# Kernel optimization log

Measured on AMD Instinct MI355X. Metric: run time of the kernel, lower is better.

The kernel has to match this reference:

```python
import jax, jax.numpy as jnp
import numpy as np
import math

DIM = 512
HEADS = 8
B = 16
P = 2048
REL_MAX = 64
REL_SIZE = 2 * REL_MAX + 1
RANK = 4
ALPHA = 16.0
QBITS = 4


def simq(w, bits=QBITS):
    # symmetric linear fake-quantization (matches simulate_quantization)
    qmin = -2 ** (bits - 1)
    qmax = 2 ** (bits - 1) - 1
    m = jnp.max(jnp.abs(w))
    scale = m / qmax
    q = jnp.clip(jnp.round(w / (scale + 1e-8)), qmin, qmax) * scale
    return jnp.where(m == 0, w, q)


def lora_lin(x, W, b, A, LB):
    # F.linear with quantized weight/bias + LoRA path
    out = x @ simq(W).T + simq(b)
    return out + (x @ A.T @ LB.T) * (ALPHA / RANK)


def setup_inputs() -> dict:
    key = jax.random.key(0)
    ks = jax.random.split(key, 20)
    d2 = DIM * 2
    inp = {
        "curr_pos": 2048,
        "z_curr_ri": jax.random.normal(ks[0], (B, DIM, 2), jnp.float32),
        "z_past_ri": jax.random.normal(ks[1], (P, B, DIM, 2), jnp.float32),
        "rel_bias_ri": jax.random.normal(ks[2], (REL_SIZE, DIM, 2), jnp.float32) * 0.02,
    }
    names = ["q", "k", "v", "o"]
    for i, n in enumerate(names):
        kw, ka, kb = jax.random.split(ks[3 + i], 3)
        inp["W" + n] = jax.random.normal(kw, (d2, d2), jnp.float32) / math.sqrt(d2)
        inp["b" + n] = jnp.zeros((d2,), jnp.float32)
        inp["A" + n] = jax.random.normal(ka, (RANK, d2), jnp.float32) / math.sqrt(d2)
        inp["LB" + n] = jax.random.normal(kb, (d2, RANK), jnp.float32) * 0.01
    return inp


def reference(curr_pos, z_curr_ri, z_past_ri, rel_bias_ri,
              Wq, bq, Aq, LBq, Wk, bk, Ak, LBk,
              Wv, bv, Av, LBv, Wo, bo, Ao, LBo):
    Bsz = z_curr_ri.shape[0]
    past_len = z_past_ri.shape[0]
    dim = z_curr_ri.shape[1]
    hd = dim // HEADS

    # projections on real-view of complex inputs ([.., dim, 2] -> [.., 2*dim])
    q = lora_lin(z_curr_ri.reshape(Bsz, dim * 2), Wq, bq, Aq, LBq)
    k = lora_lin(z_past_ri.reshape(past_len, Bsz, dim * 2), Wk, bk, Ak, LBk)
    v = lora_lin(z_past_ri.reshape(past_len, Bsz, dim * 2), Wv, bv, Av, LBv)

    q = q.reshape(Bsz, HEADS, hd, 2)            # [B,H,hd,2]
    k = k.reshape(past_len, Bsz, HEADS, hd, 2)  # [P,B,H,hd,2]
    v = v.reshape(past_len, Bsz, HEADS, hd, 2)
    qr, qi = q[..., 0], q[..., 1]
    kr, ki = k[..., 0], k[..., 1]
    vr, vi = v[..., 0], v[..., 1]

    # Re(q * conj(k)) summed over head_dim -> [B,H,P]
    dot = jnp.einsum('bhd,pbhd->bhp', qr, kr) + jnp.einsum('bhd,pbhd->bhp', qi, ki)

    # relative positional bias lookup (clamped index)
    rel_d = jnp.arange(curr_pos - past_len, curr_pos)
    idx = jnp.clip(rel_d + REL_MAX, 0, rel_bias_ri.shape[0] - 1)
    rb = rel_bias_ri[idx].reshape(past_len, HEADS, hd, 2)  # [P,H,hd,2]
    rel = jnp.einsum('bhd,phd->bhp', qr, rb[..., 0]) + jnp.einsum('bhd,phd->bhp', qi, rb[..., 1])

    w = jax.nn.softmax((dot + rel) / math.sqrt(hd), axis=-1)  # [B,H,P]

    # real softmax weights applied to complex values
    out_r = jnp.einsum('bhp,pbhd->bhd', w, vr)
    out_i = jnp.einsum('bhp,pbhd->bhd', w, vi)
    out_ri = jnp.stack([out_r, out_i], axis=-1).reshape(Bsz, dim * 2)

    o = lora_lin(out_ri, Wo, bo, Ao, LBo)
    return o.reshape(Bsz, dim, 2)  # real view of complex output [B,dim]
```

## Files before the change

kernel.cpp:

```cpp
#include <hip/hip_runtime.h>
#include <math.h>

typedef _Float16 f16;
typedef _Float16 f16x8 __attribute__((ext_vector_type(8)));
typedef _Float16 f16x4 __attribute__((ext_vector_type(4)));
typedef float f32x4 __attribute__((ext_vector_type(4)));

#define NP 2048
#define M_ROWS 32768

#define OFF_ABSMAX 0u
#define OFF_TQ     256u
#define OFF_TO     512u
#define OFF_QBIAS  1024u
#define OFF_QBUF   163840u
#define OFF_ATT    229376u
#define OFF_PM     294912u
#define OFF_PL     299008u
#define OFF_PO     303104u
#define OFF_WH     1048576u
#define OFF_TK     9437184u
#define OFF_TV     9961472u
#define OFF_KV     10485760u

__device__ __forceinline__ float qint_of(float w, float scale) {
    return fminf(7.f, fmaxf(-8.f, rintf(w / (scale + 1e-8f))));
}

__device__ __forceinline__ void gload16(const void* g, void* l) {
  __builtin_amdgcn_global_load_lds((const __attribute__((address_space(1))) void*)g,
                                   (__attribute__((address_space(3))) void*)l, 16, 0, 0);
}

__global__ void __launch_bounds__(256) absmax_kernel(
    const float* __restrict__ W0, const float* __restrict__ W1,
    const float* __restrict__ W2, const float* __restrict__ W3,
    unsigned* __restrict__ absmax) {
  int mat = blockIdx.x >> 6;
  int blk = blockIdx.x & 63;
  const float* W = mat == 0 ? W0 : mat == 1 ? W1 : mat == 2 ? W2 : W3;
  int tid = blk * 256 + threadIdx.x;
  const float4* W4 = (const float4*)W;
  float m = 0.f;
  #pragma unroll
  for (int i = 0; i < 16; ++i) {
    float4 v = W4[tid + i * 16384];
    m = fmaxf(m, fmaxf(fmaxf(fabsf(v.x), fabsf(v.y)), fmaxf(fabsf(v.z), fabsf(v.w))));
  }
  #pragma unroll
  for (int k = 32; k >= 1; k >>= 1) m = fmaxf(m, __shfl_xor(m, k));
  __shared__ float sm[4];
  if ((threadIdx.x & 63) == 0) sm[threadIdx.x >> 6] = m;
  __syncthreads();
  if (threadIdx.x == 0) {
    m = fmaxf(fmaxf(sm[0], sm[1]), fmaxf(sm[2], sm[3]));
    atomicMax(&absmax[mat], __float_as_uint(m));
  }
}

__global__ void __launch_bounds__(256) bias_quant_kernel(
    const float* __restrict__ b0, const float* __restrict__ b1,
    const float* __restrict__ b2, const float* __restrict__ b3,
    float* __restrict__ qbias) {
  int mat = blockIdx.x;
  const float* bb = mat == 0 ? b0 : mat == 1 ? b1 : mat == 2 ? b2 : b3;
  int t = threadIdx.x;
  float4 v = ((const float4*)bb)[t];
  float m = fmaxf(fmaxf(fabsf(v.x), fabsf(v.y)), fmaxf(fabsf(v.z), fabsf(v.w)));
  #pragma unroll
  for (int k = 32; k >= 1; k >>= 1) m = fmaxf(m, __shfl_xor(m, k));
  __shared__ float sm[4];
  if ((t & 63) == 0) sm[t >> 6] = m;
  __syncthreads();
  float M = fmaxf(fmaxf(sm[0], sm[1]), fmaxf(sm[2], sm[3]));
  float scale = M * (1.0f / 7.0f);
  float4 q;
  q.x = (M == 0.f) ? v.x : qint_of(v.x, scale) * scale;
  q.y = (M == 0.f) ? v.y : qint_of(v.y, scale) * scale;
  q.z = (M == 0.f) ? v.z : qint_of(v.z, scale) * scale;
  q.w = (M == 0.f) ? v.w : qint_of(v.w, scale) * scale;
  ((float4*)(qbias + mat * 1024))[t] = q;
}

__global__ void __launch_bounds__(256) quantW_kernel(
    const float* __restrict__ W0, const float* __restrict__ W1,
    const float* __restrict__ W2, const float* __restrict__ W3,
    const unsigned* __restrict__ absmax, f16* __restrict__ Wh,
    f16* __restrict__ WD) {
  int gid = blockIdx.x * 256 + threadIdx.x;
  int mat = gid >> 18;
  int idx = gid & 262143;
  const float* W = mat == 0 ? W0 : mat == 1 ? W1 : mat == 2 ? W2 : W3;
  float scale = __uint_as_float(absmax[mat]) * (1.0f / 7.0f);
  float4 v = ((const float4*)W)[idx];
  f16x4 r;
  r[0] = (f16)qint_of(v.x, scale);
  r[1] = (f16)qint_of(v.y, scale);
  r[2] = (f16)qint_of(v.z, scale);
  r[3] = (f16)qint_of(v.w, scale);
  *(f16x4*)(Wh + (size_t)mat * 1048576 + (size_t)idx * 4) = r;
  if (WD != nullptr && (mat == 1 || mat == 2)) {
    f16x8 d = {r[0], r[0], r[1], r[1], r[2], r[2], r[3], r[3]};
    int n = idx >> 8, c4 = idx & 255;
    *(f16x8*)(WD + (size_t)(mat - 1) * 2097152 + (size_t)n * 2048 + c4 * 8) = d;
  }
}

__global__ void __launch_bounds__(256) lora_t_small_kernel(
    const float* __restrict__ x, const float* __restrict__ A, float* __restrict__ t) {
  int tt = threadIdx.x;
  int b = tt >> 4;
  int r = (tt >> 2) & 3;
  int s = tt & 3;
  const float4* xv = (const float4*)(x + b * 1024 + s * 256);
  const float4* av = (const float4*)(A + r * 1024 + s * 256);
  float acc = 0.f;
  #pragma unroll 4
  for (int i = 0; i < 64; ++i) {
    float4 a = xv[i], c = av[i];
    acc += a.x * c.x + a.y * c.y + a.z * c.z + a.w * c.w;
  }
  acc += __shfl_xor(acc, 1);
  acc += __shfl_xor(acc, 2);
  if (s == 0) t[b * 4 + r] = acc;
}

__global__ void __launch_bounds__(256) lora_t_big_kernel(
    const float* __restrict__ zp, const float* __restrict__ Ak,
    const float* __restrict__ Av, float* __restrict__ tk, float* __restrict__ tv,
    f16* __restrict__ zpi) {
  __shared__ float sA[8 * 1024];
  for (int i = 0; i < 8; ++i) {
    int f4 = threadIdx.x + i * 256;
    float4 v = (f4 < 1024) ? ((const float4*)Ak)[f4] : ((const float4*)Av)[f4 - 1024];
    ((float4*)sA)[f4] = v;
  }
  __syncthreads();
  int lane = threadIdx.x & 63, wave = threadIdx.x >> 6;
  for (int it = 0; it < 4; ++it) {
    int m = blockIdx.x * 16 + wave * 4 + it;
    const float4* xr = (const float4*)(zp + (size_t)m * 1024);
    float acc[8] = {0.f, 0.f, 0.f, 0.f, 0.f, 0.f, 0.f, 0.f};
    for (int c = lane; c < 256; c += 64) {
      float4 xv = xr[c];
      if (zpi) {
        f16 h0 = (f16)xv.x, h1 = (f16)xv.y, h2 = (f16)xv.z, h3 = (f16)xv.w;
        f16x8 iv = {h0, (f16)(xv.x - (float)h0), h1, (f16)(xv.y - (float)h1),
                    h2, (f16)(xv.z - (float)h2), h3, (f16)(xv.w - (float)h3)};
        *(f16x8*)(zpi + (size_t)m * 2048 + c * 8) = iv;
      }
      #pragma unroll
      for (int r = 0; r < 8; ++r) {
        float4 a = ((const float4*)sA)[r * 256 + c];
        acc[r] += xv.x * a.x + xv.y * a.y + xv.z * a.z + xv.w * a.w;
      }
    }
    #pragma unroll
    for (int k = 32; k >= 1; k >>= 1) {
      #pragma unroll
      for (int r = 0; r < 8; ++r) acc[r] += __shfl_xor(acc[r], k);
    }
    if (lane == 0) {
      tk[m * 4 + 0] = acc[0]; tk[m * 4 + 1] = acc[1];
      tk[m * 4 + 2] = acc[2]; tk[m * 4 + 3] = acc[3];
      tv[m * 4 + 0] = acc[4]; tv[m * 4 + 1] = acc[5];
      tv[m * 4 + 2] = acc[6]; tv[m * 4 + 3] = acc[7];
    }
  }
}

__global__ void __launch_bounds__(256) gemv_mfma_kernel(
    const float* __restrict__ x, const f16* __restrict__ Wm,
    const unsigned* __restrict__ absmax, int mat,
    const float* __restrict__ qb, const float* __restrict__ t,
    const float* __restrict__ LB, float* __restrict__ out) {
  int wave = threadIdx.x >> 6, lane = threadIdx.x & 63;
  int nf = blockIdx.x * 4 + wave;
  int n0 = nf * 16;
  int row = lane & 15, kq = lane >> 4;
  f32x4 acc = {0.f, 0.f, 0.f, 0.f};
  const float* xp = x + row * 1024 + kq * 8;
  const f16* wp = Wm + (size_t)(n0 + row) * 1024 + kq * 8;
  #pragma unroll 4
  for (int k0 = 0; k0 < 1024; k0 += 32) {
    float4 a0 = *(const float4*)(xp + k0);
    float4 a1 = *(const float4*)(xp + k0 + 4);
    f16 h0 = (f16)a0.x, h1 = (f16)a0.y, h2 = (f16)a0.z, h3 = (f16)a0.w;
    f16 h4 = (f16)a1.x, h5 = (f16)a1.y, h6 = (f16)a1.z, h7 = (f16)a1.w;
    f16x8 ah = {h0, h1, h2, h3, h4, h5, h6, h7};
    f16x8 al = {(f16)(a0.x - (float)h0), (f16)(a0.y - (float)h1),
                (f16)(a0.z - (float)h2), (f16)(a0.w - (float)h3),
                (f16)(a1.x - (float)h4), (f16)(a1.y - (float)h5),
                (f16)(a1.z - (float)h6), (f16)(a1.w - (float)h7)};
    f16x8 bb = *(const f16x8*)(wp + k0);
    acc = __builtin_amdgcn_mfma_f32_16x16x32_f16(ah, bb, acc, 0, 0, 0);
    acc = __builtin_amdgcn_mfma_f32_16x16x32_f16(al, bb, acc, 0, 0, 0);
  }
  float scale = __uint_as_float(absmax[mat]) * (1.0f / 7.0f);
  int col = n0 + row;
  float bias = qb[col];
  float4 lb = *(const float4*)(LB + col * 4);
  #pragma unroll
  for (int j = 0; j < 4; ++j) {
    int m = kq * 4 + j;
    float4 tvv = *(const float4*)(t + m * 4);
    out[m * 1024 + col] =
        scale * acc[j] + bias + 4.0f * (tvv.x * lb.x + tvv.y * lb.y + tvv.z * lb.z + tvv.w * lb.w);
  }
}

__global__ void __launch_bounds__(256, 2) kv_gemm_kernel(
    const float* __restrict__ zp, const f16* __restrict__ Wh,
    const unsigned* __restrict__ absmax, const float* __restrict__ qbias,
    const float* __restrict__ tk, const float* __restrict__ tv,
    const float* __restrict__ LBk, const float* __restrict__ LBv,
    f16* __restrict__ kout, f16* __restrict__ vout) {
  __shared__ __align__(16) f16 sAh[128][40];
  __shared__ __align__(16) f16 sAl[128][40];
  __shared__ __align__(16) f16 sB[128][40];
  __shared__ float sT[128][4];

  int nb = blockIdx.x;
  int m0 = blockIdx.y * 128;
  bool is_v = nb >= 8;
  int n0 = (nb & 7) * 128;
  int mat = is_v ? 2 : 1;
  const f16* Wm = Wh + (size_t)mat * 1048576;
  const float* ttv = is_v ? tv : tk;
  const float* LBm = is_v ? LBv : LBk;
  const float* qb = qbias + mat * 1024;
  f16* outp = is_v ? vout : kout;

  int tid = threadIdx.x;
  int lane = tid & 63, wave = tid >> 6;
  int wm = (wave >> 1) * 64, wn = (wave & 1) * 64;
  int row = lane & 15, kq = lane >> 4;

  f32x4 acc[4][4];
  #pragma unroll
  for (int i = 0; i < 4; ++i)
    #pragma unroll
    for (int j = 0; j < 4; ++j) acc[i][j] = (f32x4){0.f, 0.f, 0.f, 0.f};

  int sr = tid >> 1, seg = tid & 1;
  const float* asrc = zp + (size_t)(m0 + sr) * 1024 + seg * 16;
  const f16* bsrc = Wm + (size_t)(n0 + sr) * 1024 + seg * 16;

  for (int k0 = 0; k0 < 1024; k0 += 32) {
    __syncthreads();
    float xs[16];
    const float4* a4 = (const float4*)(asrc + k0);
    *(float4*)&xs[0] = a4[0];
    *(float4*)&xs[4] = a4[1];
    *(float4*)&xs[8] = a4[2];
    *(float4*)&xs[12] = a4[3];
    f16 hs[16], ls[16];
    #pragma unroll
    for (int i = 0; i < 16; ++i) {
      f16 h = (f16)xs[i];
      hs[i] = h;
      ls[i] = (f16)(xs[i] - (float)h);
    }
    *(f16x8*)&sAh[sr][seg * 16] = *(f16x8*)&hs[0];
    *(f16x8*)&sAh[sr][seg * 16 + 8] = *(f16x8*)&hs[8];
    *(f16x8*)&sAl[sr][seg * 16] = *(f16x8*)&ls[0];
    *(f16x8*)&sAl[sr][seg * 16 + 8] = *(f16x8*)&ls[8];
    const f16x8* b8 = (const f16x8*)(bsrc + k0);
    *(f16x8*)&sB[sr][seg * 16] = b8[0];
    *(f16x8*)&sB[sr][seg * 16 + 8] = b8[1];
    __syncthreads();
    f16x8 ah[4], al[4], bf[4];
    #pragma unroll
    for (int mi = 0; mi < 4; ++mi) {
      ah[mi] = *(const f16x8*)&sAh[wm + mi * 16 + row][kq * 8];
      al[mi] = *(const f16x8*)&sAl[wm + mi * 16 + row][kq * 8];
    }
    #pragma unroll
    for (int ni = 0; ni < 4; ++ni) bf[ni] = *(const f16x8*)&sB[wn + ni * 16 + row][kq * 8];
    #pragma unroll
    for (int mi = 0; mi < 4; ++mi)
      #pragma unroll
      for (int ni = 0; ni < 4; ++ni)
        acc[mi][ni] = __builtin_amdgcn_mfma_f32_16x16x32_f16(ah[mi], bf[ni], acc[mi][ni], 0, 0, 0);
    #pragma unroll
    for (int mi = 0; mi < 4; ++mi)
      #pragma unroll
      for (int ni = 0; ni < 4; ++ni)
        acc[mi][ni] = __builtin_amdgcn_mfma_f32_16x16x32_f16(al[mi], bf[ni], acc[mi][ni], 0, 0, 0);
  }
  ((float2*)sT)[tid] = ((const float2*)(ttv + (size_t)m0 * 4))[tid];
  __syncthreads();
  float scale = __uint_as_float(absmax[mat]) * (1.0f / 7.0f);
  #pragma unroll
  for (int ni = 0; ni < 4; ++ni) {
    int ncol = n0 + wn + ni * 16 + row;
    int h = ncol >> 7, d = ncol & 127;
    float4 lb = *(const float4*)(LBm + ncol * 4);
    float bias = qb[ncol];
    #pragma unroll
    for (int mi = 0; mi < 4; ++mi) {
      #pragma unroll
      for (int j = 0; j < 4; ++j) {
        int mloc = wm + mi * 16 + kq * 4 + j;
        int m = m0 + mloc;
        int p = m >> 4, b = m & 15;
        float4 t4 = *(const float4*)&sT[mloc][0];
        float val = scale * acc[mi][ni][j] + bias +
                    4.0f * (t4.x * lb.x + t4.y * lb.y + t4.z * lb.z + t4.w * lb.w);
        outp[(((size_t)(b * 8 + h)) * 2048 + p) * 128 + d] = (f16)val;
      }
    }
  }
}

__global__ void __launch_bounds__(256, 2) kv_gemm_fast_kernel(
    const f16* __restrict__ zpi, const f16* __restrict__ WD,
    const unsigned* __restrict__ absmax, const float* __restrict__ qbias,
    const float* __restrict__ tk, const float* __restrict__ tv,
    const float* __restrict__ LBk, const float* __restrict__ LBv,
    f16* __restrict__ kout, f16* __restrict__ vout) {
  __shared__ __align__(16) f16 sbuf[32768];
  __shared__ float sT[128][4];

  int linear = blockIdx.x + (blockIdx.y << 4);
  int xcd = linear & 7;
  int slot = linear >> 3;
  int nb = slot & 15;
  int g = ((slot >> 4) << 3) + xcd;
  int m0 = g << 7;

  bool is_v = nb >= 8;
  int n0 = (nb & 7) * 128;
  int mat = is_v ? 2 : 1;
  int h = nb & 7;
  const float* ttv = is_v ? tv : tk;
  const float* LBm = is_v ? LBv : LBk;
  const float* qb = qbias + mat * 1024;
  f16* outp = is_v ? vout : kout;

  int tid = threadIdx.x;
  int lane = tid & 63, wave = tid >> 6;
  int wm = (wave >> 1) * 64, wn = (wave & 1) * 64;
  int row = lane & 15, kq = lane >> 4;

  const f16* srcA = zpi + (size_t)m0 * 2048;
  const f16* srcB = WD + (size_t)(is_v ? 1 : 0) * 2097152 + (size_t)n0 * 2048;

  int goff[4], lbase[4];
  #pragma unroll
  for (int r = 0; r < 4; ++r) {
    int L = r * 256 + tid;
    int rw = L >> 3, cc = L & 7, cs = cc ^ (rw & 7);
    goff[r] = rw * 2048 + cs * 8;
    lbase[r] = r * 2048 + wave * 512;
  }

  f32x4 acc[4][4];
  #pragma unroll
  for (int i = 0; i < 4; ++i)
    #pragma unroll
    for (int j = 0; j < 4; ++j) acc[i][j] = (f32x4){0.f, 0.f, 0.f, 0.f};

  int radA[8], radB[8];
  #pragma unroll
  for (int mi = 0; mi < 4; ++mi) {
    int Ra = wm + mi * 16 + row;
    int Rb = wn + mi * 16 + row;
    #pragma unroll
    for (int ks = 0; ks < 2; ++ks) {
      radA[mi * 2 + ks] = Ra * 64 + (((ks * 4 + kq) ^ (Ra & 7)) << 3);
      radB[mi * 2 + ks] = Rb * 64 + (((ks * 4 + kq) ^ (Rb & 7)) << 3);
    }
  }

  #pragma unroll
  for (int r = 0; r < 4; ++r) {
    gload16(srcA + goff[r], sbuf + lbase[r]);
    gload16(srcB + goff[r], sbuf + 8192 + lbase[r]);
  }
  __syncthreads();

  int cur = 0;
  for (int t = 0; t < 32; ++t) {
    if (t < 31) {
      int nxt = (cur ^ 1) * 16384;
      int gk = (t + 1) * 64;
      #pragma unroll
      for (int r = 0; r < 4; ++r) {
        gload16(srcA + goff[r] + gk, sbuf + nxt + lbase[r]);
        gload16(srcB + goff[r] + gk, sbuf + nxt + 8192 + lbase[r]);
      }
    }
    const f16* bA = sbuf + cur * 16384;
    const f16* bB = bA + 8192;
    f16x8 af[8], bf[8];
    #pragma unroll
    for (int i = 0; i < 8; ++i) {
      af[i] = *(const f16x8*)&bA[radA[i]];
      bf[i] = *(const f16x8*)&bB[radB[i]];
    }
    #pragma unroll
    for (int ks = 0; ks < 2; ++ks)
      #pragma unroll
      for (int mi = 0; mi < 4; ++mi)
        #pragma unroll
        for (int ni = 0; ni < 4; ++ni)
          acc[mi][ni] = __builtin_amdgcn_mfma_f32_16x16x32_f16(
              af[mi * 2 + ks], bf[ni * 2 + ks], acc[mi][ni], 0, 0, 0);
    __syncthreads();
    cur ^= 1;
  }

  ((float2*)sT)[tid] = ((const float2*)(ttv + (size_t)m0 * 4))[tid];
  __syncthreads();
  float scale = __uint_as_float(absmax[mat]) * (1.0f / 7.0f);
  float biasv[4];
  float4 lbv[4];
  #pragma unroll
  for (int ni = 0; ni < 4; ++ni) {
    int ncol = n0 + wn + ni * 16 + row;
    biasv[ni] = qb[ncol];
    lbv[ni] = *(const float4*)(LBm + ncol * 4);
  }
  float* tbuf = (float*)sbuf;
  int lh = lane >> 5, l5 = lane & 31;
  #pragma unroll
  for (int halfsel = 0; halfsel < 2; ++halfsel) {
    __syncthreads();
    if ((wave >> 1) == halfsel) {
      #pragma unroll
      for (int ni = 0; ni < 4; ++ni) {
        #pragma unroll
        for (int mi = 0; mi < 4; ++mi) {
          #pragma unroll
          for (int j = 0; j < 4; ++j) {
            int ml = mi * 16 + kq * 4 + j;
            float4 t4 = *(const float4*)&sT[wm + ml][0];
            tbuf[ml * 132 + wn + ni * 16 + row] =
                scale * acc[mi][ni][j] + biasv[ni] +
                4.0f * (t4.x * lbv[ni].x + t4.y * lbv[ni].y + t4.z * lbv[ni].z +
                        t4.w * lbv[ni].w);
          }
        }
      }
    }
    __syncthreads();
    #pragma unroll
    for (int it = 0; it < 8; ++it) {
      int ml = it * 8 + wave * 2 + lh;
      int m = m0 + halfsel * 64 + ml;
      int p = m >> 4, b = m & 15;
      float4 v = *(const float4*)&tbuf[ml * 132 + l5 * 4];
      f16x4 hv = {(f16)v.x, (f16)v.y, (f16)v.z, (f16)v.w};
      *(f16x4*)(outp + (((size_t)(b * 8 + h)) * 2048 + p) * 128 + l5 * 4) = hv;
    }
  }
}

__device__ __forceinline__ float4 ld4h(const f16* p) {
  f16x4 v = *reinterpret_cast<const f16x4*>(p);
  return make_float4((float)v[0], (float)v[1], (float)v[2], (float)v[3]);
}

__global__ void __launch_bounds__(256) attn_part_kernel(
    const float* __restrict__ qbuf, const f16* __restrict__ kbuf,
    const f16* __restrict__ vbuf, const float* __restrict__ rel_bias,
    const int* __restrict__ curr_pos_p, float* __restrict__ m_part,
    float* __restrict__ l_part, float* __restrict__ o_part) {
  __shared__ float sS[256];
  __shared__ float red[8];
  __shared__ float sOv[8][132];
  int bh = blockIdx.x;
  int c = blockIdx.y;
  int b = bh >> 3, h = bh & 7;
  int p0 = c * 256;
  int tid = threadIdx.x, lane = tid & 63, wave = tid >> 6;
  int j4 = lane & 31, ph = lane >> 5;
  float4 qv = *(const float4*)(qbuf + b * 1024 + h * 128 + j4 * 4);
  int off = *curr_pos_p - NP + 64;
  const f16* kb = kbuf + ((size_t)bh * 2048 + p0) * 128;
  for (int i = 0; i < 32; ++i) {
    int pl = i * 8 + wave * 2 + ph;
    float4 kv = ld4h(kb + (size_t)pl * 128 + j4 * 4);
    int idx = min(max(p0 + pl + off, 0), 128);
    float4 rb = *(const float4*)(rel_bias + idx * 1024 + h * 128 + j4 * 4);
    float a = qv.x * (kv.x + rb.x) + qv.y * (kv.y + rb.y) +
              qv.z * (kv.z + rb.z) + qv.w * (kv.w + rb.w);
    a += __shfl_xor(a, 16);
    a += __shfl_xor(a, 8);
    a += __shfl_xor(a, 4);
    a += __shfl_xor(a, 2);
    a += __shfl_xor(a, 1);
    if (j4 == 0) sS[pl] = a * 0.125f;
  }
  __syncthreads();
  float v = sS[tid];
  float mx = v;
  #pragma unroll
  for (int k = 32; k >= 1; k >>= 1) mx = fmaxf(mx, __shfl_xor(mx, k));
  if (lane == 0) red[wave] = mx;
  __syncthreads();
  mx = fmaxf(fmaxf(red[0], red[1]), fmaxf(red[2], red[3]));
  float e = expf(v - mx);
  sS[tid] = e;
  float sum = e;
  #pragma unroll
  for (int k = 32; k >= 1; k >>= 1) sum += __shfl_xor(sum, k);
  if (lane == 0) red[4 + wave] = sum;
  __syncthreads();
  float l = red[4] + red[5] + red[6] + red[7];
  int d4 = tid & 31, pg = tid >> 5;
  const f16* vb = vbuf + ((size_t)bh * 2048 + p0 + pg * 32) * 128;
  float4 a4 = make_float4(0.f, 0.f, 0.f, 0.f);
  #pragma unroll 4
  for (int i = 0; i < 32; ++i) {
    float s = sS[pg * 32 + i];
    float4 vv = ld4h(vb + (size_t)i * 128 + d4 * 4);
    a4.x += s * vv.x;
    a4.y += s * vv.y;
    a4.z += s * vv.z;
    a4.w += s * vv.w;
  }
  *(float4*)&sOv[pg][d4 * 4] = a4;
  __syncthreads();
  if (tid < 128) {
    float o = 0.f;
    #pragma unroll
    for (int gI = 0; gI < 8; ++gI) o += sOv[gI][tid];
    int pc = bh * 8 + c;
    o_part[pc * 128 + tid] = o;
    if (tid == 0) {
      m_part[pc] = mx;
      l_part[pc] = l;
    }
  }
}

__global__ void __launch_bounds__(128) attn_combine_kernel(
    const float* __restrict__ m_part, const float* __restrict__ l_part,
    const float* __restrict__ o_part, float* __restrict__ attout) {
  int bh = blockIdx.x;
  int d = threadIdx.x;
  float M = -1e30f;
  #pragma unroll
  for (int c = 0; c < 8; ++c) M = fmaxf(M, m_part[bh * 8 + c]);
  float L = 0.f, o = 0.f;
  #pragma unroll
  for (int c = 0; c < 8; ++c) {
    float w = expf(m_part[bh * 8 + c] - M);
    L += w * l_part[bh * 8 + c];
    o += w * o_part[(bh * 8 + c) * 128 + d];
  }
  int b = bh >> 3, h = bh & 7;
  attout[b * 1024 + h * 128 + d] = o / L;
}

extern "C" void kernel_launch(void* const* d_in, const int* in_sizes, int n_in,
                              void* d_out, int out_size, void* d_ws, size_t ws_size,
                              hipStream_t stream) {
  const int* curr_pos = (const int*)d_in[0];
  const float* z_curr = (const float*)d_in[1];
  const float* z_past = (const float*)d_in[2];
  const float* rel_bias = (const float*)d_in[3];
  const float* Wq = (const float*)d_in[4];
  const float* bq = (const float*)d_in[5];
  const float* Aq = (const float*)d_in[6];
  const float* LBq = (const float*)d_in[7];
  const float* Wk = (const float*)d_in[8];
  const float* bk = (const float*)d_in[9];
  const float* Ak = (const float*)d_in[10];
  const float* LBk = (const float*)d_in[11];
  const float* Wv = (const float*)d_in[12];
  const float* bv = (const float*)d_in[13];
  const float* Av = (const float*)d_in[14];
  const float* LBv = (const float*)d_in[15];
  const float* Wo = (const float*)d_in[16];
  const float* bo = (const float*)d_in[17];
  const float* Ao = (const float*)d_in[18];
  const float* LBo = (const float*)d_in[19];

  char* ws = (char*)d_ws;
  unsigned* absmax = (unsigned*)(ws + OFF_ABSMAX);
  float* t_q = (float*)(ws + OFF_TQ);
  float* t_o = (float*)(ws + OFF_TO);
  float* qbias = (float*)(ws + OFF_QBIAS);
  float* qbuf = (float*)(ws + OFF_QBUF);
  float* attout = (float*)(ws + OFF_ATT);
  float* pm = (float*)(ws + OFF_PM);
  float* pl = (float*)(ws + OFF_PL);
  float* po = (float*)(ws + OFF_PO);
  f16* Wh = (f16*)(ws + OFF_WH);
  float* t_k = (float*)(ws + OFF_TK);
  float* t_v = (float*)(ws + OFF_TV);
  char* kvbase = ws + OFF_KV;

  f16* kb = (f16*)kvbase;
  f16* vb = (f16*)(kvbase + 67108864ull);
  f16* zpi = (f16*)(kvbase + 134217728ull);
  f16* WD = (f16*)(kvbase + 268435456ull);
  bool fast = ws_size >= (size_t)OFF_KV + 276824064ull;

  hipMemsetAsync(absmax, 0, 16, stream);
  absmax_kernel<<<256, 256, 0, stream>>>(Wq, Wk, Wv, Wo, absmax);
  bias_quant_kernel<<<4, 256, 0, stream>>>(bq, bk, bv, bo, qbias);
  quantW_kernel<<<4096, 256, 0, stream>>>(Wq, Wk, Wv, Wo, absmax, Wh,
                                          fast ? WD : nullptr);
  lora_t_small_kernel<<<1, 256, 0, stream>>>(z_curr, Aq, t_q);
  gemv_mfma_kernel<<<16, 256, 0, stream>>>(z_curr, Wh, absmax, 0, qbias, t_q, LBq, qbuf);
  lora_t_big_kernel<<<2048, 256, 0, stream>>>(z_past, Ak, Av, t_k, t_v,
                                              fast ? zpi : nullptr);
  if (fast)
    kv_gemm_fast_kernel<<<dim3(16, 256), 256, 0, stream>>>(
        zpi, WD, absmax, qbias, t_k, t_v, LBk, LBv, kb, vb);
  else
    kv_gemm_kernel<<<dim3(16, 256), 256, 0, stream>>>(
        z_past, Wh, absmax, qbias, t_k, t_v, LBk, LBv, kb, vb);
  attn_part_kernel<<<dim3(128, 8), 256, 0, stream>>>(
      qbuf, kb, vb, rel_bias, curr_pos, pm, pl, po);
  attn_combine_kernel<<<128, 128, 0, stream>>>(pm, pl, po, attout);
  lora_t_small_kernel<<<1, 256, 0, stream>>>(attout, Ao, t_o);
  gemv_mfma_kernel<<<16, 256, 0, stream>>>(attout, Wh + 3ull * 1048576ull, absmax, 3,
                                           qbias + 3 * 1024, t_o, LBo, (float*)d_out);
}
```

Baseline: 753.0 us.

## Split z_past into hi/lo planes and use 32x32 MFMA with 128x256 KV tiles

```diff
diff --git a/kernel.cpp b/kernel.cpp
--- a/kernel.cpp
+++ b/kernel.cpp
@@ -5,6 +5,7 @@
 typedef _Float16 f16x8 __attribute__((ext_vector_type(8)));
 typedef _Float16 f16x4 __attribute__((ext_vector_type(4)));
 typedef float f32x4 __attribute__((ext_vector_type(4)));
+typedef float f32x16 __attribute__((ext_vector_type(16)));
 
 #define NP 2048
 #define M_ROWS 32768
@@ -85,8 +86,7 @@
 __global__ void __launch_bounds__(256) quantW_kernel(
     const float* __restrict__ W0, const float* __restrict__ W1,
     const float* __restrict__ W2, const float* __restrict__ W3,
-    const unsigned* __restrict__ absmax, f16* __restrict__ Wh,
-    f16* __restrict__ WD) {
+    const unsigned* __restrict__ absmax, f16* __restrict__ Wh) {
   int gid = blockIdx.x * 256 + threadIdx.x;
   int mat = gid >> 18;
   int idx = gid & 262143;
@@ -99,11 +99,6 @@
   r[2] = (f16)qint_of(v.z, scale);
   r[3] = (f16)qint_of(v.w, scale);
   *(f16x4*)(Wh + (size_t)mat * 1048576 + (size_t)idx * 4) = r;
-  if (WD != nullptr && (mat == 1 || mat == 2)) {
-    f16x8 d = {r[0], r[0], r[1], r[1], r[2], r[2], r[3], r[3]};
-    int n = idx >> 8, c4 = idx & 255;
-    *(f16x8*)(WD + (size_t)(mat - 1) * 2097152 + (size_t)n * 2048 + c4 * 8) = d;
-  }
 }
 
 __global__ void __launch_bounds__(256) lora_t_small_kernel(
@@ -128,7 +123,7 @@
 __global__ void __launch_bounds__(256) lora_t_big_kernel(
     const float* __restrict__ zp, const float* __restrict__ Ak,
     const float* __restrict__ Av, float* __restrict__ tk, float* __restrict__ tv,
-    f16* __restrict__ zpi) {
+    f16* __restrict__ zph, f16* __restrict__ zpl) {
   __shared__ float sA[8 * 1024];
   for (int i = 0; i < 8; ++i) {
     int f4 = threadIdx.x + i * 256;
@@ -143,11 +138,13 @@
     float acc[8] = {0.f, 0.f, 0.f, 0.f, 0.f, 0.f, 0.f, 0.f};
     for (int c = lane; c < 256; c += 64) {
       float4 xv = xr[c];
-      if (zpi) {
+      if (zph) {
         f16 h0 = (f16)xv.x, h1 = (f16)xv.y, h2 = (f16)xv.z, h3 = (f16)xv.w;
-        f16x8 iv = {h0, (f16)(xv.x - (float)h0), h1, (f16)(xv.y - (float)h1),
-                    h2, (f16)(xv.z - (float)h2), h3, (f16)(xv.w - (float)h3)};
-        *(f16x8*)(zpi + (size_t)m * 2048 + c * 8) = iv;
+        f16x4 hv = {h0, h1, h2, h3};
+        f16x4 lv = {(f16)(xv.x - (float)h0), (f16)(xv.y - (float)h1),
+                    (f16)(xv.z - (float)h2), (f16)(xv.w - (float)h3)};
+        *(f16x4*)(zph + (size_t)m * 1024 + c * 4) = hv;
+        *(f16x4*)(zpl + (size_t)m * 1024 + c * 4) = lv;
       }
       #pragma unroll
       for (int r = 0; r < 8; ++r) {
@@ -314,25 +311,25 @@
 }
 
 __global__ void __launch_bounds__(256, 2) kv_gemm_fast_kernel(
-    const f16* __restrict__ zpi, const f16* __restrict__ WD,
-    const unsigned* __restrict__ absmax, const float* __restrict__ qbias,
-    const float* __restrict__ tk, const float* __restrict__ tv,
-    const float* __restrict__ LBk, const float* __restrict__ LBv,
-    f16* __restrict__ kout, f16* __restrict__ vout) {
+    const f16* __restrict__ zph, const f16* __restrict__ zpl,
+    const f16* __restrict__ Wh, const unsigned* __restrict__ absmax,
+    const float* __restrict__ qbias, const float* __restrict__ tk,
+    const float* __restrict__ tv, const float* __restrict__ LBk,
+    const float* __restrict__ LBv, f16* __restrict__ kout, f16* __restrict__ vout) {
   __shared__ __align__(16) f16 sbuf[32768];
   __shared__ float sT[128][4];
 
-  int linear = blockIdx.x + (blockIdx.y << 4);
+  int linear = blockIdx.x + (blockIdx.y << 3);
   int xcd = linear & 7;
-  int slot = linear >> 3;
-  int nb = slot & 15;
-  int g = ((slot >> 4) << 3) + xcd;
+  int q = linear >> 3;
+  int nb = q & 7;
+  int g = ((q >> 3) << 3) + xcd;
   int m0 = g << 7;
 
-  bool is_v = nb >= 8;
-  int n0 = (nb & 7) * 128;
+  bool is_v = nb >= 4;
+  int n0 = (nb & 3) * 256;
   int mat = is_v ? 2 : 1;
-  int h = nb & 7;
+  const f16* Wm = Wh + (size_t)mat * 1048576;
   const float* ttv = is_v ? tv : tk;
   const float* LBm = is_v ? LBv : LBk;
   const float* qb = qbias + mat * 1024;
@@ -340,73 +337,90 @@
 
   int tid = threadIdx.x;
   int lane = tid & 63, wave = tid >> 6;
-  int wm = (wave >> 1) * 64, wn = (wave & 1) * 64;
-  int row = lane & 15, kq = lane >> 4;
-
-  const f16* srcA = zpi + (size_t)m0 * 2048;
-  const f16* srcB = WD + (size_t)(is_v ? 1 : 0) * 2097152 + (size_t)n0 * 2048;
-
-  int goff[4], lbase[4];
+  int wm = (wave & 1) * 64;
+  int wn = (wave >> 1) * 128;
+  int l31 = lane & 31, kh = lane >> 5;
+
+  const f16* srcAh = zph + (size_t)m0 * 1024;
+  const f16* srcAl = zpl + (size_t)m0 * 1024;
+  const f16* srcB = Wm + (size_t)n0 * 1024;
+
+  int gA[2], gB[4];
+  #pragma unroll
+  for (int r = 0; r < 2; ++r) {
+    int L = r * 256 + tid;
+    gA[r] = (L & 127) * 1024 + (L >> 7) * 8;
+  }
   #pragma unroll
   for (int r = 0; r < 4; ++r) {
     int L = r * 256 + tid;
-    int rw = L >> 3, cc = L & 7, cs = cc ^ (rw & 7);
-    goff[r] = rw * 2048 + cs * 8;
-    lbase[r] = r * 2048 + wave * 512;
-  }
-
-  f32x4 acc[4][4];
-  #pragma unroll
-  for (int i = 0; i < 4; ++i)
-    #pragma unroll
-    for (int j = 0; j < 4; ++j) acc[i][j] = (f32x4){0.f, 0.f, 0.f, 0.f};
-
-  int radA[8], radB[8];
-  #pragma unroll
-  for (int mi = 0; mi < 4; ++mi) {
-    int Ra = wm + mi * 16 + row;
-    int Rb = wn + mi * 16 + row;
-    #pragma unroll
-    for (int ks = 0; ks < 2; ++ks) {
-      radA[mi * 2 + ks] = Ra * 64 + (((ks * 4 + kq) ^ (Ra & 7)) << 3);
-      radB[mi * 2 + ks] = Rb * 64 + (((ks * 4 + kq) ^ (Rb & 7)) << 3);
-    }
-  }
-
-  #pragma unroll
-  for (int r = 0; r < 4; ++r) {
-    gload16(srcA + goff[r], sbuf + lbase[r]);
-    gload16(srcB + goff[r], sbuf + 8192 + lbase[r]);
-  }
+    gB[r] = (L & 255) * 1024 + (L >> 8) * 8;
+  }
+  int ldsA = wave * 512;
+  int ldsB = wave * 512;
+
+  f32x16 acc[2][4];
+  #pragma unroll
+  for (int i = 0; i < 2; ++i)
+    #pragma unroll
+    for (int j = 0; j < 4; ++j)
+      #pragma unroll
+      for (int e = 0; e < 16; ++e) acc[i][j][e] = 0.f;
+
+  int radA[2][2], radB[4][2];
+  #pragma unroll
+  for (int ks = 0; ks < 2; ++ks) {
+    int c = ks * 2 + kh;
+    #pragma unroll
+    for (int ri = 0; ri < 2; ++ri)
+      radA[ri][ks] = (c * 128 + wm + ri * 32 + l31) * 8;
+    #pragma unroll
+    for (int ci = 0; ci < 4; ++ci)
+      radB[ci][ks] = 8192 + (c * 256 + wn + ci * 32 + l31) * 8;
+  }
+
+  #pragma unroll
+  for (int r = 0; r < 2; ++r) {
+    gload16(srcAh + gA[r], sbuf + r * 2048 + ldsA);
+    gload16(srcAl + gA[r], sbuf + 4096 + r * 2048 + ldsA);
+  }
+  #pragma unroll
+  for (int r = 0; r < 4; ++r) gload16(srcB + gB[r], sbuf + 8192 + r * 2048 + ldsB);
   __syncthreads();
 
   int cur = 0;
   for (int t = 0; t < 32; ++t) {
     if (t < 31) {
       int nxt = (cur ^ 1) * 16384;
-      int gk = (t + 1) * 64;
-      #pragma unroll
-      for (int r = 0; r < 4; ++r) {
-        gload16(srcA + goff[r] + gk, sbuf + nxt + lbase[r]);
-        gload16(srcB + goff[r] + gk, sbuf + nxt + 8192 + lbase[r]);
+      int gk = (t + 1) * 32;
+      #pragma unroll
+      for (int r = 0; r < 2; ++r) {
+        gload16(srcAh + gA[r] + gk, sbuf + nxt + r * 2048 + ldsA);
+        gload16(srcAl + gA[r] + gk, sbuf + nxt + 4096 + r * 2048 + ldsA);
       }
-    }
-    const f16* bA = sbuf + cur * 16384;
-    const f16* bB = bA + 8192;
-    f16x8 af[8], bf[8];
-    #pragma unroll
-    for (int i = 0; i < 8; ++i) {
-      af[i] = *(const f16x8*)&bA[radA[i]];
-      bf[i] = *(const f16x8*)&bB[radB[i]];
-    }
-    #pragma unroll
-    for (int ks = 0; ks < 2; ++ks)
-      #pragma unroll
-      for (int mi = 0; mi < 4; ++mi)
+      #pragma unroll
+      for (int r = 0; r < 4; ++r)
+        gload16(srcB + gB[r] + gk, sbuf + nxt + 8192 + r * 2048 + ldsB);
+    }
+    const f16* ph = sbuf + cur * 16384;
+    #pragma unroll
+    for (int ks = 0; ks < 2; ++ks) {
+      f16x8 ah[2], al[2], bf[4];
+      #pragma unroll
+      for (int ri = 0; ri < 2; ++ri) {
+        ah[ri] = *(const f16x8*)&ph[radA[ri][ks]];
+        al[ri] = *(const f16x8*)&ph[radA[ri][ks] + 4096];
+      }
+      #pragma unroll
+      for (int ci = 0; ci < 4; ++ci) bf[ci] = *(const f16x8*)&ph[radB[ci][ks]];
+      #pragma unroll
+      for (int ci = 0; ci < 4; ++ci)
         #pragma unroll
-        for (int ni = 0; ni < 4; ++ni)
-          acc[mi][ni] = __builtin_amdgcn_mfma_f32_16x16x32_f16(
-              af[mi * 2 + ks], bf[ni * 2 + ks], acc[mi][ni], 0, 0, 0);
+        for (int ri = 0; ri < 2; ++ri) {
+          acc[ri][ci] = __builtin_amdgcn_mfma_f32_32x32x16_f16(ah[ri], bf[ci], acc[ri][ci], 0, 0, 0);
+          acc[ri][ci] = __builtin_amdgcn_mfma_f32_32x32x16_f16(al[ri], bf[ci], acc[ri][ci], 0, 0, 0);
+        }
+    }
     __syncthreads();
     cur ^= 1;
   }
@@ -417,29 +431,28 @@
   float biasv[4];
   float4 lbv[4];
   #pragma unroll
-  for (int ni = 0; ni < 4; ++ni) {
-    int ncol = n0 + wn + ni * 16 + row;
-    biasv[ni] = qb[ncol];
-    lbv[ni] = *(const float4*)(LBm + ncol * 4);
-  }
-  float* tbuf = (float*)sbuf;
-  int lh = lane >> 5, l5 = lane & 31;
-  #pragma unroll
-  for (int halfsel = 0; halfsel < 2; ++halfsel) {
+  for (int ci = 0; ci < 4; ++ci) {
+    int ncol = n0 + wn + ci * 32 + l31;
+    biasv[ci] = qb[ncol];
+    lbv[ci] = *(const float4*)(LBm + ncol * 4);
+  }
+  f16* tbuf = sbuf;
+  #pragma unroll
+  for (int h2 = 0; h2 < 2; ++h2) {
     __syncthreads();
-    if ((wave >> 1) == halfsel) {
-      #pragma unroll
-      for (int ni = 0; ni < 4; ++ni) {
+    if ((wave & 1) == h2) {
+      #pragma unroll
+      for (int ri = 0; ri < 2; ++ri) {
         #pragma unroll
-        for (int mi = 0; mi < 4; ++mi) {
+        for (int ci = 0; ci < 4; ++ci) {
           #pragma unroll
-          for (int j = 0; j < 4; ++j) {
-            int ml = mi * 16 + kq * 4 + j;
-            float4 t4 = *(const float4*)&sT[wm + ml][0];
-            tbuf[ml * 132 + wn + ni * 16 + row] =
-                scale * acc[mi][ni][j] + biasv[ni] +
-                4.0f * (t4.x * lbv[ni].x + t4.y * lbv[ni].y + t4.z * lbv[ni].z +
-                        t4.w * lbv[ni].w);
+          for (int j = 0; j < 16; ++j) {
+            int rowl = ri * 32 + (j & 3) + 8 * (j >> 2) + 4 * kh;
+            float4 t4 = *(const float4*)&sT[h2 * 64 + rowl][0];
+            float vv = scale * acc[ri][ci][j] + biasv[ci] +
+                       4.0f * (t4.x * lbv[ci].x + t4.y * lbv[ci].y +
+                               t4.z * lbv[ci].z + t4.w * lbv[ci].w);
+            tbuf[rowl * 264 + wn + ci * 32 + l31] = (f16)vv;
           }
         }
       }
@@ -447,12 +460,13 @@
     __syncthreads();
     #pragma unroll
     for (int it = 0; it < 8; ++it) {
-      int ml = it * 8 + wave * 2 + lh;
-      int m = m0 + halfsel * 64 + ml;
+      int I = it * 256 + tid;
+      int r = I >> 5, c8 = I & 31;
+      int m = m0 + h2 * 64 + r;
       int p = m >> 4, b = m & 15;
-      float4 v = *(const float4*)&tbuf[ml * 132 + l5 * 4];
-      f16x4 hv = {(f16)v.x, (f16)v.y, (f16)v.z, (f16)v.w};
-      *(f16x4*)(outp + (((size_t)(b * 8 + h)) * 2048 + p) * 128 + l5 * 4) = hv;
+      int hh = (nb & 3) * 2 + (c8 >> 4);
+      f16x8 v = *(const f16x8*)&tbuf[r * 264 + c8 * 8];
+      *(f16x8*)(outp + (((size_t)(b * 8 + hh)) * 2048 + p) * 128 + (c8 & 15) * 8) = v;
     }
   }
 }
@@ -596,22 +610,21 @@
 
   f16* kb = (f16*)kvbase;
   f16* vb = (f16*)(kvbase + 67108864ull);
-  f16* zpi = (f16*)(kvbase + 134217728ull);
-  f16* WD = (f16*)(kvbase + 268435456ull);
-  bool fast = ws_size >= (size_t)OFF_KV + 276824064ull;
+  f16* zph = (f16*)(kvbase + 134217728ull);
+  f16* zpl = (f16*)(kvbase + 201326592ull);
+  bool fast = ws_size >= (size_t)OFF_KV + 268435456ull;
 
   hipMemsetAsync(absmax, 0, 16, stream);
   absmax_kernel<<<256, 256, 0, stream>>>(Wq, Wk, Wv, Wo, absmax);
   bias_quant_kernel<<<4, 256, 0, stream>>>(bq, bk, bv, bo, qbias);
-  quantW_kernel<<<4096, 256, 0, stream>>>(Wq, Wk, Wv, Wo, absmax, Wh,
-                                          fast ? WD : nullptr);
+  quantW_kernel<<<4096, 256, 0, stream>>>(Wq, Wk, Wv, Wo, absmax, Wh);
   lora_t_small_kernel<<<1, 256, 0, stream>>>(z_curr, Aq, t_q);
   gemv_mfma_kernel<<<16, 256, 0, stream>>>(z_curr, Wh, absmax, 0, qbias, t_q, LBq, qbuf);
   lora_t_big_kernel<<<2048, 256, 0, stream>>>(z_past, Ak, Av, t_k, t_v,
-                                              fast ? zpi : nullptr);
+                                              fast ? zph : nullptr, fast ? zpl : nullptr);
   if (fast)
-    kv_gemm_fast_kernel<<<dim3(16, 256), 256, 0, stream>>>(
-        zpi, WD, absmax, qbias, t_k, t_v, LBk, LBv, kb, vb);
+    kv_gemm_fast_kernel<<<dim3(8, 256), 256, 0, stream>>>(
+        zph, zpl, Wh, absmax, qbias, t_k, t_v, LBk, LBv, kb, vb);
   else
     kv_gemm_kernel<<<dim3(16, 256), 256, 0, stream>>>(
         z_past, Wh, absmax, qbias, t_k, t_v, LBk, LBv, kb, vb);
```

Result: slower. 802.6 us (+6.6%).
